# Kernel tuning notes

Hardware: AMD Instinct MI355X
Metric: run time of the kernel (lower is better)

The kernel has to match this reference:

```python
import jax, jax.numpy as jnp
import numpy as np


def setup_inputs() -> dict:
    key = jax.random.key(0)
    k1, k2 = jax.random.split(key)
    z = jax.random.normal(k1, (16, 128, 32, 32), dtype=jnp.float32)
    codes = jax.random.normal(k2, (8, 512, 16), dtype=jnp.float32)  # [latent_dim, num_codes, channel_dim]
    return {"z": z, "codes": codes}


def reference(z, codes):
    L, K, D = codes.shape          # latent_dim, num_codes, channel_dim
    B, C, H, W = z.shape           # C == L * D
    # permute to channels-last and split channels into (L, D)
    h = jnp.transpose(z, (0, 2, 3, 1)).reshape(B, H, W, L, D)
    # pairwise L2 distances via ||h||^2 - 2 h.W + ||W||^2 (avoids materializing [B,H,W,L,K,D])
    h2 = jnp.sum(h * h, axis=-1)                      # [B,H,W,L]
    w2 = jnp.sum(codes * codes, axis=-1)              # [L,K]
    cross = jnp.einsum('bhwld,lkd->bhwlk', h, codes)  # [B,H,W,L,K]
    d2 = h2[..., None] - 2.0 * cross + w2[None, None, None]
    distances = jnp.sqrt(jnp.maximum(d2, 1e-12))      # [B,H,W,L,K]
    # softmin over codes == softmax of negated distances
    probs = jax.nn.softmax(-distances, axis=4)
    soft_symbols = jnp.einsum('bhwlk,lkd->bhwld', probs, codes).reshape(B, H, W, C)
    # hard assignment: nearest code per latent dim
    idxes = jnp.argmin(distances, axis=4)             # [B,H,W,L]
    hard_symbols = codes[jnp.arange(L), idxes]        # [B,H,W,L,D]
    hard_symbols = hard_symbols.reshape(B, H, W, C)
    return (soft_symbols, hard_symbols, idxes)
```

## Files before the change

### kernel.cpp

```cpp
#include <hip/hip_runtime.h>
#include <hip/hip_bf16.h>

typedef float  f32x4  __attribute__((ext_vector_type(4)));
typedef short  s16x8  __attribute__((ext_vector_type(8)));
typedef __bf16 bf16x8 __attribute__((ext_vector_type(8)));

namespace {
constexpr int BHW = 16384, L = 8, K = 512, D = 16, HW = 1024, CH = 128;
constexpr int TPB = 512;
constexpr int PPB = 256;
constexpr float KAPPA = 2.0813689810056077f;
constexpr size_t WS_CA_BYTES = (size_t)L * K * 32 * 2;
constexpr size_t WS_W2_BYTES = (size_t)L * K * 4;
constexpr size_t WS_W2K_OFF  = WS_CA_BYTES + WS_W2_BYTES;

__device__ __forceinline__ f32x4 mfma16(s16x8 a, s16x8 b, f32x4 c) {
  return __builtin_amdgcn_mfma_f32_16x16x32_bf16(
      __builtin_bit_cast(bf16x8, a), __builtin_bit_cast(bf16x8, b), c, 0, 0, 0);
}
__device__ __forceinline__ unsigned short bfh(float x) {
  return __builtin_bit_cast(unsigned short, __float2bfloat16(x));
}
__device__ __forceinline__ float bf2f(unsigned short u) {
  return __bfloat162float(__builtin_bit_cast(__hip_bfloat16, u));
}

__global__ void repack(const float* __restrict__ codes,
                       unsigned short* __restrict__ cA,
                       float* __restrict__ w2g, float* __restrict__ w2k) {
  int i = blockIdx.x * 256 + threadIdx.x;
  const float* c = codes + (size_t)i * D;
  float s = 0.f;
  #pragma unroll
  for (int d = 0; d < D; ++d) s = fmaf(c[d], c[d], s);
  w2g[i] = s;
  w2k[i] = KAPPA * s;
  int l = i >> 9, k = i & (K - 1);
  int ck = k >> 5, kloc = k & 31, g = kloc >> 3, w = kloc & 7, t = w >> 2, r = w & 3;
  int prow = ck * 32 + t * 16 + g * 4 + r;
  unsigned short* dst = cA + ((size_t)l * K + prow) * 32;
  #pragma unroll
  for (int d = 0; d < D; ++d) {
    unsigned short hi = bfh(c[d]);
    dst[d] = hi; dst[16 + d] = bfh(c[d] - bf2f(hi));
  }
}

__global__ __launch_bounds__(TPB, 4) void enc_mfma(
    const float* __restrict__ z,
    const float* __restrict__ codes,
    const unsigned short* __restrict__ cA,
    const float* __restrict__ w2g,
    const float* __restrict__ w2k,
    float* __restrict__ out)
{
  __shared__ short cB[2][8192];
  __shared__ short cAl[16384];
  __shared__ float w2s[K];
  __shared__ float h2s[PPB];
  __shared__ float ssum[8][32];
  __shared__ int   bks[8][32];

  const int tid  = threadIdx.x;
  const int l    = blockIdx.y;
  const int bx   = blockIdx.x;
  const int bimg = bx >> 2;
  const int yx0  = (bx & 3) * PPB;

  float* hstg = (float*)&cB[0][0];
  {
    const int i = tid & 255, dc = tid >> 8;
    #pragma unroll
    for (int it = 0; it < 8; ++it) {
      int d = dc * 8 + it;
      hstg[i * 17 + d] = z[((size_t)(bimg * CH + l * D + d)) * HW + yx0 + i];
    }
  }
  {
    const s16x8* src = (const s16x8*)(cA + ((size_t)l * K + tid) * 32);
    s16x8* dst = (s16x8*)cAl + tid * 4;
    dst[0] = src[0]; dst[1] = src[1]; dst[2] = src[2]; dst[3] = src[3];
  }
  __syncthreads();

  const int wv   = __builtin_amdgcn_readfirstlane(tid >> 6);
  const int lane = tid & 63;
  const int cl   = lane & 15;
  const int g    = lane >> 4;
  const int pw   = wv * 32;

  if (tid < PPB) {
    float h2 = 0.f;
    #pragma unroll
    for (int d = 0; d < 16; ++d) { float v = hstg[tid * 17 + d]; h2 = fmaf(v, v, h2); }
    h2s[tid] = h2;
  }
  s16x8 B1a, B2a, B1b, B2b;
  {
    const int off = (g & 1) * 8;
    #pragma unroll
    for (int j = 0; j < 8; ++j) {
      float va = hstg[(pw + cl) * 17 + off + j];
      unsigned short ha = bfh(va);
      B1a[j] = (short)ha; B2a[j] = (short)bfh(va - bf2f(ha));
      float vb = hstg[(pw + 16 + cl) * 17 + off + j];
      unsigned short hb = bfh(vb);
      B1b[j] = (short)hb; B2b[j] = (short)bfh(vb - bf2f(hb));
    }
  }
  __syncthreads();
  const float h2ka = KAPPA * h2s[pw + cl];
  const float h2kb = KAPPA * h2s[pw + 16 + cl];

  {
    int k = tid, ck = k >> 5, kloc = k & 31, gg = kloc >> 3, w = kloc & 7, t = w >> 2, r = w & 3;
    int prow = ck * 32 + t * 16 + gg * 4 + r;
    const s16x8* src = (const s16x8*)(cA + ((size_t)l * K + prow) * 32);
    s16x8 h0 = src[0], h1 = src[1], l0 = src[2], l1 = src[3];
    int base = (ck * 4 + gg) * 128 + w;
    #pragma unroll
    for (int d = 0; d < 8; ++d) {
      cB[0][base + d * 8]       = h0[d];
      cB[1][base + d * 8]       = l0[d];
      cB[0][base + (d + 8) * 8] = h1[d];
      cB[1][base + (d + 8) * 8] = l1[d];
    }
    w2s[k] = w2k[l * K + k];
  }
  __syncthreads();

  const s16x8* Abl = (const s16x8*)cAl + (cl * 4 + g);
  const s16x8 ONES = {(short)0x3F80, (short)0x3F80, (short)0x3F80, (short)0x3F80,
                      (short)0x3F80, (short)0x3F80, (short)0x3F80, (short)0x3F80};

  float m2A = 1e30f, mbA = 1e30f;
  float m2B = 1e30f, mbB = 1e30f;
  f32x4 pva0 = {0,0,0,0}, pva1 = {0,0,0,0}, pvsA = {0,0,0,0};
  f32x4 pvb0 = {0,0,0,0}, pvb1 = {0,0,0,0}, pvsB = {0,0,0,0};

  auto soft8 = [&](const f32x4& T0, const f32x4& T1, const f32x4& W0, const f32x4& W1,
                   float h2k, int ct, float& m2, float& m2b) -> s16x8 {
    s16x8 PA;
    #pragma unroll
    for (int t = 0; t < 2; ++t) {
      #pragma unroll
      for (int r = 0; r < 4; ++r) {
        float T  = t ? T1[r] : T0[r];
        float Wk = t ? W1[r] : W0[r];
        float d2 = fmaf(-2.f * KAPPA, T, h2k) + Wk;
        d2 = fmaxf(d2, 1e-12f);
        int kloc = ct * 32 + 8 * g + t * 4 + r;
        float key = __int_as_float((__float_as_int(d2) & 0xFFFFFE00) | kloc);
        m2b = __builtin_amdgcn_fmed3f(key, m2, m2b);
        m2  = fminf(m2, key);
        float dist = __builtin_amdgcn_sqrtf(d2);
        float w = __builtin_amdgcn_exp2f(-dist);
        PA[t * 4 + r] = (short)bfh(w);
      }
    }
    return PA;
  };

  #pragma unroll 2
  for (int ct = 0; ct < 16; ++ct) {
    s16x8 A0 = Abl[ct * 128];
    s16x8 A1 = Abl[ct * 128 + 64];
    s16x8 Bh = *(const s16x8*)&cB[0][(ct * 4 + g) * 128 + cl * 8];
    s16x8 Bl = *(const s16x8*)&cB[1][(ct * 4 + g) * 128 + cl * 8];
    f32x4 W0 = *(const f32x4*)&w2s[ct * 32 + 8 * g];
    f32x4 W1 = *(const f32x4*)&w2s[ct * 32 + 8 * g + 4];

    f32x4 T0a = {0,0,0,0}, T1a = {0,0,0,0}, T0b = {0,0,0,0}, T1b = {0,0,0,0};
    __builtin_amdgcn_s_setprio(1);
    T0a = mfma16(A0, B1a, T0a); T0a = mfma16(A0, B2a, T0a);
    T1a = mfma16(A1, B1a, T1a); T1a = mfma16(A1, B2a, T1a);
    T0b = mfma16(A0, B1b, T0b); T0b = mfma16(A0, B2b, T0b);
    T1b = mfma16(A1, B1b, T1b); T1b = mfma16(A1, B2b, T1b);
    __builtin_amdgcn_s_setprio(0);

    s16x8 PAa = soft8(T0a, T1a, W0, W1, h2ka, ct, m2A, mbA);
    s16x8 PAb = soft8(T0b, T1b, W0, W1, h2kb, ct, m2B, mbB);
    __builtin_amdgcn_s_setprio(1);
    pva0 = mfma16(PAa, Bh, pva0); pva1 = mfma16(PAa, Bl, pva1); pvsA = mfma16(PAa, ONES, pvsA);
    pvb0 = mfma16(PAb, Bh, pvb0); pvb1 = mfma16(PAb, Bl, pvb1); pvsB = mfma16(PAb, ONES, pvsB);
    __builtin_amdgcn_s_setprio(0);
  }
  f32x4 pva = pva0 + pva1;
  f32x4 pvb = pvb0 + pvb1;

  #pragma unroll
  for (int off = 16; off < 64; off <<= 1) {
    float mo = __shfl_xor(m2A, off), mbo = __shfl_xor(mbA, off);
    mbA = fminf(fminf(mbA, mbo), fmaxf(m2A, mo));
    m2A = fminf(m2A, mo);
    float mo2 = __shfl_xor(m2B, off), mbo2 = __shfl_xor(mbB, off);
    mbB = fminf(fminf(mbB, mbo2), fmaxf(m2B, mo2));
    m2B = fminf(m2B, mo2);
  }
  int kaA = __float_as_int(m2A) & 511;
  int kaB = __float_as_int(m2B) & 511;
  bool trigA = (__int_as_float(__float_as_int(mbA) & 0xFFFFFE00) -
                __int_as_float(__float_as_int(m2A) & 0xFFFFFE00)) < 0.045f;
  bool trigB = (__int_as_float(__float_as_int(mbB) & 0xFFFFFE00) -
                __int_as_float(__float_as_int(m2B) & 0xFFFFFE00)) < 0.045f;

  if (cl == 0) {
    #pragma unroll
    for (int r = 0; r < 4; ++r) {
      ssum[wv][g * 4 + r]      = pvsA[r];
      ssum[wv][16 + g * 4 + r] = pvsB[r];
    }
  }
  if (lane < 16) { bks[wv][lane] = kaA; bks[wv][16 + lane] = kaB; }

  unsigned long long mask = __ballot(lane < 16 && trigA) |
                            (__ballot(lane < 16 && trigB) << 16);
  while (mask) {
    int pl = __ffsll((long long)mask) - 1; mask &= mask - 1;
    float hh[16];
    #pragma unroll
    for (int d = 0; d < 16; ++d)
      hh[d] = z[((size_t)(bimg * CH + l * D + d)) * HW + yx0 + pw + pl];
    float h2x = h2s[pw + pl];
    float bm = 1e30f; int bkk = 0;
    for (int rnd = 0; rnd < 8; ++rnd) {
      int k = rnd * 64 + lane;
      const float* cr = codes + ((size_t)l * K + k) * D;
      float cross = 0.f;
      #pragma unroll
      for (int d = 0; d < 16; ++d) cross = fmaf(hh[d], cr[d], cross);
      float d2 = (h2x - 2.f * cross) + w2g[l * K + k];
      d2 = fmaxf(d2, 1e-12f);
      float dist = sqrtf(d2);
      if (dist < bm) { bm = dist; bkk = k; }
    }
    #pragma unroll
    for (int off = 1; off < 64; off <<= 1) {
      float bo = __shfl_xor(bm, off); int ko = __shfl_xor(bkk, off);
      if (bo < bm || (bo == bm && ko < bkk)) { bm = bo; bkk = ko; }
    }
    if (lane == 0) bks[wv][pl] = bkk;
  }

  __syncthreads();
  const int pg0 = bimg * HW + yx0;
  f32x4 svA = *(const f32x4*)&ssum[wv][g * 4];
  f32x4 svB = *(const f32x4*)&ssum[wv][16 + g * 4];
  #pragma unroll
  for (int r = 0; r < 4; ++r) {
    out[(size_t)(pg0 + pw + g * 4 + r) * CH + l * D + cl]      = pva[r] * __builtin_amdgcn_rcpf(svA[r]);
    out[(size_t)(pg0 + pw + 16 + g * 4 + r) * CH + l * D + cl] = pvb[r] * __builtin_amdgcn_rcpf(svB[r]);
  }
  int kkA = bks[wv][cl];
  int kkB = bks[wv][16 + cl];
  float4 cvA = *(const float4*)&codes[((size_t)l * K + kkA) * D + g * 4];
  float4 cvB = *(const float4*)&codes[((size_t)l * K + kkB) * D + g * 4];
  *(float4*)&out[(size_t)BHW * CH + (size_t)(pg0 + pw + cl) * CH + l * D + g * 4]      = cvA;
  *(float4*)&out[(size_t)BHW * CH + (size_t)(pg0 + pw + 16 + cl) * CH + l * D + g * 4] = cvB;
  if (lane < 16) {
    out[(size_t)2 * BHW * CH + (size_t)(pg0 + pw + cl) * L + l]      = (float)kkA;
    out[(size_t)2 * BHW * CH + (size_t)(pg0 + pw + 16 + cl) * L + l] = (float)kkB;
  }
}
}

extern "C" void kernel_launch(void* const* d_in, const int* in_sizes, int n_in,
                              void* d_out, int out_size, void* d_ws, size_t ws_size,
                              hipStream_t stream) {
  const float* z     = (const float*)d_in[0];
  const float* codes = (const float*)d_in[1];
  float* out         = (float*)d_out;
  unsigned short* cA = (unsigned short*)d_ws;
  float* w2g         = (float*)((char*)d_ws + WS_CA_BYTES);
  float* w2k         = (float*)((char*)d_ws + WS_W2K_OFF);

  repack<<<dim3(L * K / 256), 256, 0, stream>>>(codes, cA, w2g, w2k);
  dim3 grid(BHW / PPB, L);
  enc_mfma<<<grid, TPB, 0, stream>>>(z, codes, cA, w2g, w2k, out);
}
```

Baseline: 61.24 us.

## Split code dimension across wave halves, halve pixels per block, drop LDS code copy

Each block now handles 128 pixels instead of 256. The two halves of the 8 waves each process half of the 512 codes for the same pixels, and partial softmax sums, weighted-code accumulators and top-2 minima are merged through LDS. The per-block LDS copy of the packed code matrix is removed and A fragments are read straight from global/L2. The aim is more blocks in flight and less LDS use per block, at the cost of an extra cross-half reduction, extra barriers and repeated global loads of the code fragments.

New measurement: 74.66 us. +21.9%, slower.

```diff
diff --git a/kernel.cpp b/kernel.cpp
--- a/kernel.cpp
+++ b/kernel.cpp
@@ -8,7 +8,7 @@
 namespace {
 constexpr int BHW = 16384, L = 8, K = 512, D = 16, HW = 1024, CH = 128;
 constexpr int TPB = 512;
-constexpr int PPB = 256;
+constexpr int PPB = 128;
 constexpr float KAPPA = 2.0813689810056077f;
 constexpr size_t WS_CA_BYTES = (size_t)L * K * 32 * 2;
 constexpr size_t WS_W2_BYTES = (size_t)L * K * 4;
@@ -55,31 +55,24 @@
     float* __restrict__ out)
 {
   __shared__ short cB[2][8192];
-  __shared__ short cAl[16384];
   __shared__ float w2s[K];
   __shared__ float h2s[PPB];
-  __shared__ float ssum[8][32];
-  __shared__ int   bks[8][32];
+  __shared__ int   bks[4][32];
 
   const int tid  = threadIdx.x;
   const int l    = blockIdx.y;
   const int bx   = blockIdx.x;
-  const int bimg = bx >> 2;
-  const int yx0  = (bx & 3) * PPB;
+  const int bimg = bx >> 3;
+  const int yx0  = (bx & 7) * PPB;
 
   float* hstg = (float*)&cB[0][0];
   {
-    const int i = tid & 255, dc = tid >> 8;
-    #pragma unroll
-    for (int it = 0; it < 8; ++it) {
-      int d = dc * 8 + it;
+    const int i = tid & 127, dc = tid >> 7;
+    #pragma unroll
+    for (int it = 0; it < 4; ++it) {
+      int d = dc * 4 + it;
       hstg[i * 17 + d] = z[((size_t)(bimg * CH + l * D + d)) * HW + yx0 + i];
     }
-  }
-  {
-    const s16x8* src = (const s16x8*)(cA + ((size_t)l * K + tid) * 32);
-    s16x8* dst = (s16x8*)cAl + tid * 4;
-    dst[0] = src[0]; dst[1] = src[1]; dst[2] = src[2]; dst[3] = src[3];
   }
   __syncthreads();
 
@@ -87,7 +80,9 @@
   const int lane = tid & 63;
   const int cl   = lane & 15;
   const int g    = lane >> 4;
-  const int pw   = wv * 32;
+  const int pgp  = wv & 3;
+  const int half = wv >> 2;
+  const int pw   = pgp * 32;
 
   if (tid < PPB) {
     float h2 = 0.f;
@@ -129,7 +124,7 @@
   }
   __syncthreads();
 
-  const s16x8* Abl = (const s16x8*)cAl + (cl * 4 + g);
+  const s16x8* Ab = (const s16x8*)(cA + (size_t)l * K * 32) + (cl * 4 + g);
   const s16x8 ONES = {(short)0x3F80, (short)0x3F80, (short)0x3F80, (short)0x3F80,
                       (short)0x3F80, (short)0x3F80, (short)0x3F80, (short)0x3F80};
 
@@ -161,10 +156,12 @@
     return PA;
   };
 
+  const int ck0 = half * 8;
   #pragma unroll 2
-  for (int ct = 0; ct < 16; ++ct) {
-    s16x8 A0 = Abl[ct * 128];
-    s16x8 A1 = Abl[ct * 128 + 64];
+  for (int cki = 0; cki < 8; ++cki) {
+    const int ct = ck0 + cki;
+    s16x8 A0 = Ab[ct * 128];
+    s16x8 A1 = Ab[ct * 128 + 64];
     s16x8 Bh = *(const s16x8*)&cB[0][(ct * 4 + g) * 128 + cl * 8];
     s16x8 Bl = *(const s16x8*)&cB[1][(ct * 4 + g) * 128 + cl * 8];
     f32x4 W0 = *(const f32x4*)&w2s[ct * 32 + 8 * g];
@@ -197,69 +194,102 @@
     mbB = fminf(fminf(mbB, mbo2), fmaxf(m2B, mo2));
     m2B = fminf(m2B, mo2);
   }
-  int kaA = __float_as_int(m2A) & 511;
-  int kaB = __float_as_int(m2B) & 511;
-  bool trigA = (__int_as_float(__float_as_int(mbA) & 0xFFFFFE00) -
-                __int_as_float(__float_as_int(m2A) & 0xFFFFFE00)) < 0.045f;
-  bool trigB = (__int_as_float(__float_as_int(mbB) & 0xFFFFFE00) -
-                __int_as_float(__float_as_int(m2B) & 0xFFFFFE00)) < 0.045f;
-
-  if (cl == 0) {
+
+  float* pvbuf = (float*)&cB[0][0];
+  float* svbuf = pvbuf + 128 * 17;
+  float* smbuf = svbuf + 128;
+  __syncthreads();
+  if (half == 1) {
     #pragma unroll
     for (int r = 0; r < 4; ++r) {
-      ssum[wv][g * 4 + r]      = pvsA[r];
-      ssum[wv][16 + g * 4 + r] = pvsB[r];
-    }
-  }
-  if (lane < 16) { bks[wv][lane] = kaA; bks[wv][16 + lane] = kaB; }
-
-  unsigned long long mask = __ballot(lane < 16 && trigA) |
-                            (__ballot(lane < 16 && trigB) << 16);
-  while (mask) {
-    int pl = __ffsll((long long)mask) - 1; mask &= mask - 1;
-    float hh[16];
-    #pragma unroll
-    for (int d = 0; d < 16; ++d)
-      hh[d] = z[((size_t)(bimg * CH + l * D + d)) * HW + yx0 + pw + pl];
-    float h2x = h2s[pw + pl];
-    float bm = 1e30f; int bkk = 0;
-    for (int rnd = 0; rnd < 8; ++rnd) {
-      int k = rnd * 64 + lane;
-      const float* cr = codes + ((size_t)l * K + k) * D;
-      float cross = 0.f;
+      pvbuf[(pw + g * 4 + r) * 17 + cl]      = pva[r];
+      pvbuf[(pw + 16 + g * 4 + r) * 17 + cl] = pvb[r];
+    }
+    if (cl == 0) {
       #pragma unroll
-      for (int d = 0; d < 16; ++d) cross = fmaf(hh[d], cr[d], cross);
-      float d2 = (h2x - 2.f * cross) + w2g[l * K + k];
-      d2 = fmaxf(d2, 1e-12f);
-      float dist = sqrtf(d2);
-      if (dist < bm) { bm = dist; bkk = k; }
-    }
-    #pragma unroll
-    for (int off = 1; off < 64; off <<= 1) {
-      float bo = __shfl_xor(bm, off); int ko = __shfl_xor(bkk, off);
-      if (bo < bm || (bo == bm && ko < bkk)) { bm = bo; bkk = ko; }
-    }
-    if (lane == 0) bks[wv][pl] = bkk;
-  }
-
-  __syncthreads();
-  const int pg0 = bimg * HW + yx0;
-  f32x4 svA = *(const f32x4*)&ssum[wv][g * 4];
-  f32x4 svB = *(const f32x4*)&ssum[wv][16 + g * 4];
-  #pragma unroll
-  for (int r = 0; r < 4; ++r) {
-    out[(size_t)(pg0 + pw + g * 4 + r) * CH + l * D + cl]      = pva[r] * __builtin_amdgcn_rcpf(svA[r]);
-    out[(size_t)(pg0 + pw + 16 + g * 4 + r) * CH + l * D + cl] = pvb[r] * __builtin_amdgcn_rcpf(svB[r]);
-  }
-  int kkA = bks[wv][cl];
-  int kkB = bks[wv][16 + cl];
-  float4 cvA = *(const float4*)&codes[((size_t)l * K + kkA) * D + g * 4];
-  float4 cvB = *(const float4*)&codes[((size_t)l * K + kkB) * D + g * 4];
-  *(float4*)&out[(size_t)BHW * CH + (size_t)(pg0 + pw + cl) * CH + l * D + g * 4]      = cvA;
-  *(float4*)&out[(size_t)BHW * CH + (size_t)(pg0 + pw + 16 + cl) * CH + l * D + g * 4] = cvB;
-  if (lane < 16) {
-    out[(size_t)2 * BHW * CH + (size_t)(pg0 + pw + cl) * L + l]      = (float)kkA;
-    out[(size_t)2 * BHW * CH + (size_t)(pg0 + pw + 16 + cl) * L + l] = (float)kkB;
+      for (int r = 0; r < 4; ++r) {
+        svbuf[pw + g * 4 + r]      = pvsA[r];
+        svbuf[pw + 16 + g * 4 + r] = pvsB[r];
+      }
+    }
+    if (lane < 16) {
+      smbuf[(pw + cl) * 2 + 0] = m2A;  smbuf[(pw + cl) * 2 + 1] = mbA;
+      smbuf[(pw + 16 + cl) * 2 + 0] = m2B;  smbuf[(pw + 16 + cl) * 2 + 1] = mbB;
+    }
+  }
+  __syncthreads();
+  if (half == 0) {
+    f32x4 svA, svB;
+    #pragma unroll
+    for (int r = 0; r < 4; ++r) {
+      pva[r] += pvbuf[(pw + g * 4 + r) * 17 + cl];
+      pvb[r] += pvbuf[(pw + 16 + g * 4 + r) * 17 + cl];
+      svA[r] = pvsA[r] + svbuf[pw + g * 4 + r];
+      svB[r] = pvsB[r] + svbuf[pw + 16 + g * 4 + r];
+    }
+    {
+      const float mj = smbuf[(pw + cl) * 2 + 0], mbj = smbuf[(pw + cl) * 2 + 1];
+      mbA = fminf(fminf(mbA, mbj), fmaxf(m2A, mj));
+      m2A = fminf(m2A, mj);
+      const float mj2 = smbuf[(pw + 16 + cl) * 2 + 0], mbj2 = smbuf[(pw + 16 + cl) * 2 + 1];
+      mbB = fminf(fminf(mbB, mbj2), fmaxf(m2B, mj2));
+      m2B = fminf(m2B, mj2);
+    }
+
+    int kaA = __float_as_int(m2A) & 511;
+    int kaB = __float_as_int(m2B) & 511;
+    bool trigA = (__int_as_float(__float_as_int(mbA) & 0xFFFFFE00) -
+                  __int_as_float(__float_as_int(m2A) & 0xFFFFFE00)) < 0.045f;
+    bool trigB = (__int_as_float(__float_as_int(mbB) & 0xFFFFFE00) -
+                  __int_as_float(__float_as_int(m2B) & 0xFFFFFE00)) < 0.045f;
+
+    if (lane < 16) { bks[pgp][lane] = kaA; bks[pgp][16 + lane] = kaB; }
+
+    unsigned long long mask = __ballot(lane < 16 && trigA) |
+                              (__ballot(lane < 16 && trigB) << 16);
+    while (mask) {
+      int pl = __ffsll((long long)mask) - 1; mask &= mask - 1;
+      float hh[16];
+      #pragma unroll
+      for (int d = 0; d < 16; ++d)
+        hh[d] = z[((size_t)(bimg * CH + l * D + d)) * HW + yx0 + pw + pl];
+      float h2x = h2s[pw + pl];
+      float bm = 1e30f; int bkk = 0;
+      for (int rnd = 0; rnd < 8; ++rnd) {
+        int k = rnd * 64 + lane;
+        const float* cr = codes + ((size_t)l * K + k) * D;
+        float cross = 0.f;
+        #pragma unroll
+        for (int d = 0; d < 16; ++d) cross = fmaf(hh[d], cr[d], cross);
+        float d2 = (h2x - 2.f * cross) + w2g[l * K + k];
+        d2 = fmaxf(d2, 1e-12f);
+        float dist = sqrtf(d2);
+        if (dist < bm) { bm = dist; bkk = k; }
+      }
+      #pragma unroll
+      for (int off = 1; off < 64; off <<= 1) {
+        float bo = __shfl_xor(bm, off); int ko = __shfl_xor(bkk, off);
+        if (bo < bm || (bo == bm && ko < bkk)) { bm = bo; bkk = ko; }
+      }
+      if (lane == 0) bks[pgp][pl] = bkk;
+    }
+
+    const int pg0 = bimg * HW + yx0;
+    #pragma unroll
+    for (int r = 0; r < 4; ++r) {
+      out[(size_t)(pg0 + pw + g * 4 + r) * CH + l * D + cl]      = pva[r] * __builtin_amdgcn_rcpf(svA[r]);
+      out[(size_t)(pg0 + pw + 16 + g * 4 + r) * CH + l * D + cl] = pvb[r] * __builtin_amdgcn_rcpf(svB[r]);
+    }
+    int kkA = bks[pgp][cl];
+    int kkB = bks[pgp][16 + cl];
+    float4 cvA = *(const float4*)&codes[((size_t)l * K + kkA) * D + g * 4];
+    float4 cvB = *(const float4*)&codes[((size_t)l * K + kkB) * D + g * 4];
+    *(float4*)&out[(size_t)BHW * CH + (size_t)(pg0 + pw + cl) * CH + l * D + g * 4]      = cvA;
+    *(float4*)&out[(size_t)BHW * CH + (size_t)(pg0 + pw + 16 + cl) * CH + l * D + g * 4] = cvB;
+    if (lane < 16) {
+      out[(size_t)2 * BHW * CH + (size_t)(pg0 + pw + cl) * L + l]      = (float)kkA;
+      out[(size_t)2 * BHW * CH + (size_t)(pg0 + pw + 16 + cl) * L + l] = (float)kkB;
+    }
   }
 }
 }
```
